# Kernel tuning notes

Measured on AMD Instinct MI355X. Metric: run time of the kernel, lower is better.

Reference implementation:

```python
import jax, jax.numpy as jnp
import numpy as np

WEIGHT_MSE = 1.0 / 3.0
W_DNA, W_RNA, W_LIG = 5.0, 5.0, 10.0
EPS = 1e-6


def _weighted_rigid_align(x, x_target, w):
    # x, x_target: [..., N, 3]; w: [..., N]. Aligns x onto x_target (Kabsch).
    w3 = w[..., None]                                   # [..., N, 1]
    wsum = jnp.sum(w, axis=-1, keepdims=True)[..., None]  # [..., 1, 1]
    mu_x = jnp.sum(w3 * x, axis=-2, keepdims=True) / wsum
    mu_t = jnp.sum(w3 * x_target, axis=-2, keepdims=True) / wsum
    xc = x - mu_x
    tc = x_target - mu_t
    # weighted covariance H = sum_n w_n * tc_n tc? -> [..., 3, 3]
    H = jnp.einsum('...ni,...nj->...ij', w3 * tc, xc)
    U, _, Vt = jnp.linalg.svd(H)
    d = jnp.sign(jnp.linalg.det(U @ Vt))                # reflection fix
    D = jnp.stack([jnp.ones_like(d), jnp.ones_like(d), d], axis=-1)
    R = (U * D[..., None, :]) @ Vt                      # [..., 3, 3]
    return jnp.einsum('...ij,...nj->...ni', R, xc) + mu_t


def setup_inputs() -> dict:
    key = jax.random.key(0)
    ks = jax.random.split(key, 7)
    B, S, N = 8, 48, 8192
    pred = jax.random.normal(ks[0], (B, S, N, 3), dtype=jnp.float32)
    true = jax.random.normal(ks[1], (B, N, 3), dtype=jnp.float32)
    mask = jax.random.randint(ks[2], (B, N), 0, 2, dtype=jnp.int32)
    is_dna = jax.random.randint(ks[3], (B, N), 0, 2, dtype=jnp.int32)
    is_rna = jax.random.randint(ks[4], (B, N), 0, 2, dtype=jnp.int32)
    is_lig = jax.random.randint(ks[5], (B, N), 0, 2, dtype=jnp.int32)
    scale = jax.random.uniform(ks[6], (B, S), dtype=jnp.float32)
    return {"pred_coordinate": pred, "true_coordinate": true,
            "coordinate_mask": mask, "is_dna": is_dna, "is_rna": is_rna,
            "is_ligand": is_lig, "per_sample_scale": scale}


def reference(pred_coordinate, true_coordinate, coordinate_mask, is_dna,
              is_rna, is_ligand, per_sample_scale):
    S = pred_coordinate.shape[-3]
    mask = coordinate_mask.astype(jnp.float32)          # [B, N]
    weight = (1.0 + W_DNA * is_dna.astype(jnp.float32)
              + W_RNA * is_rna.astype(jnp.float32)
              + W_LIG * is_ligand.astype(jnp.float32)) * mask
    true_m = true_coordinate * mask[..., None]          # [B, N, 3]
    pred_m = pred_coordinate * mask[..., None, :, None]  # [B, S, N, 3]
    true_e = jnp.broadcast_to(true_m[..., None, :, :], pred_coordinate.shape)
    weight_e = jnp.broadcast_to(weight[..., None, :],
                                pred_coordinate.shape[:-1])  # [B, S, N]
    aligned = jax.lax.stop_gradient(
        _weighted_rigid_align(true_e, pred_m, weight_e))
    weight_e = jax.lax.stop_gradient(weight_e)
    per_atom_se = jnp.sum((pred_coordinate - aligned) ** 2, axis=-1)  # [B,S,N]
    denom = jnp.sum(mask, axis=-1, keepdims=True) + EPS               # [B,1]
    per_sample = jnp.sum(weight_e * per_atom_se, axis=-1) / denom     # [B,S]
    per_sample = per_sample * per_sample_scale
    loss_b = WEIGHT_MSE * jnp.mean(per_sample, axis=-1)               # [B]
    return jnp.mean(loss_b)
```

## Files before the change

### kernel.cpp

```cpp
#include <hip/hip_runtime.h>
#include <math.h>

namespace {

constexpr int NB = 8;
constexpr int NS = 48;
constexpr int NA = 8192;
constexpr int BSIZE = 256;


template <int CNT>
__device__ inline void blockReduceWrite(const float (&v)[CNT], float* __restrict__ dst,
                                        float* lds, int nwaves) {
  const int lane = threadIdx.x & 63;
  const int wave = threadIdx.x >> 6;
#pragma unroll
  for (int k = 0; k < CNT; ++k) {
    float x = v[k];
#pragma unroll
    for (int off = 32; off; off >>= 1) x += __shfl_xor(x, off, 64);
    if (lane == 0) lds[wave * CNT + k] = x;
  }
  __syncthreads();
  if ((int)threadIdx.x < CNT) {
    float s = 0.f;
    for (int w = 0; w < nwaves; ++w) s += lds[w * CNT + threadIdx.x];
    dst[threadIdx.x] = s;
  }
}

__global__ __launch_bounds__(BSIZE) void reduce_kernel(
    const float* __restrict__ pred, const float* __restrict__ truec,
    const int* __restrict__ mask, const int* __restrict__ dna,
    const int* __restrict__ rna, const int* __restrict__ lig,
    float* __restrict__ ws) {
  __shared__ float lds[(BSIZE / 64) * 13];
  const int blk = blockIdx.x;

  if (blk < NB * NS) {
    const int b = blk / NS;
    const float* p = pred + (size_t)blk * NA * 3;
    const float* t = truec + (size_t)b * NA * 3;
    const int base = b * NA;

    float acc[13];
#pragma unroll
    for (int k = 0; k < 13; ++k) acc[k] = 0.f;

    auto atom = [&](float w, float p0, float p1, float p2, float t0, float t1, float t2) {
      const float w0 = w * p0, w1 = w * p1, w2 = w * p2;
      acc[0] += w0 * p0 + w1 * p1 + w2 * p2;
      acc[1] += w0;
      acc[2] += w1;
      acc[3] += w2;
      acc[4] += w0 * t0;
      acc[5] += w0 * t1;
      acc[6] += w0 * t2;
      acc[7] += w1 * t0;
      acc[8] += w1 * t1;
      acc[9] += w1 * t2;
      acc[10] += w2 * t0;
      acc[11] += w2 * t1;
      acc[12] += w2 * t2;
    };
    auto wgt = [](int m, int d, int r, int l) {
      return (1.0f + 5.0f * (float)d + 5.0f * (float)r + 10.0f * (float)l) * (float)m;
    };

    for (int it = 0; it < NA / (BSIZE * 4); ++it) {
      const int n0 = it * BSIZE * 4 + threadIdx.x * 4;
      const float4 pa = *(const float4*)(p + 3 * n0);
      const float4 pb = *(const float4*)(p + 3 * n0 + 4);
      const float4 pc = *(const float4*)(p + 3 * n0 + 8);
      const float4 ta = *(const float4*)(t + 3 * n0);
      const float4 tb = *(const float4*)(t + 3 * n0 + 4);
      const float4 tc = *(const float4*)(t + 3 * n0 + 8);
      const int4 mk = *(const int4*)(mask + base + n0);
      const int4 dn = *(const int4*)(dna + base + n0);
      const int4 rn = *(const int4*)(rna + base + n0);
      const int4 lg = *(const int4*)(lig + base + n0);

      atom(wgt(mk.x, dn.x, rn.x, lg.x), pa.x, pa.y, pa.z, ta.x, ta.y, ta.z);
      atom(wgt(mk.y, dn.y, rn.y, lg.y), pa.w, pb.x, pb.y, ta.w, tb.x, tb.y);
      atom(wgt(mk.z, dn.z, rn.z, lg.z), pb.z, pb.w, pc.x, tb.z, tb.w, tc.x);
      atom(wgt(mk.w, dn.w, rn.w, lg.w), pc.y, pc.z, pc.w, tc.y, tc.z, tc.w);
    }
    blockReduceWrite<13>(acc, ws + 64 + blk * 16, lds, BSIZE / 64);
  } else {
    const int b = blk - NB * NS;
    const float* t = truec + (size_t)b * NA * 3;
    const int base = b * NA;

    float acc[6];
#pragma unroll
    for (int k = 0; k < 6; ++k) acc[k] = 0.f;

    auto atomb = [&](int m, int d, int r, int l, float t0, float t1, float t2) {
      const float mf = (float)m;
      const float w = (1.0f + 5.0f * (float)d + 5.0f * (float)r + 10.0f * (float)l) * mf;
      acc[0] += w;
      acc[1] += w * t0;
      acc[2] += w * t1;
      acc[3] += w * t2;
      acc[4] += w * (t0 * t0 + t1 * t1 + t2 * t2);
      acc[5] += mf;
    };

    for (int it = 0; it < NA / (BSIZE * 4); ++it) {
      const int n0 = it * BSIZE * 4 + threadIdx.x * 4;
      const float4 ta = *(const float4*)(t + 3 * n0);
      const float4 tb = *(const float4*)(t + 3 * n0 + 4);
      const float4 tc = *(const float4*)(t + 3 * n0 + 8);
      const int4 mk = *(const int4*)(mask + base + n0);
      const int4 dn = *(const int4*)(dna + base + n0);
      const int4 rn = *(const int4*)(rna + base + n0);
      const int4 lg = *(const int4*)(lig + base + n0);

      atomb(mk.x, dn.x, rn.x, lg.x, ta.x, ta.y, ta.z);
      atomb(mk.y, dn.y, rn.y, lg.y, ta.w, tb.x, tb.y);
      atomb(mk.z, dn.z, rn.z, lg.z, tb.z, tb.w, tc.x);
      atomb(mk.w, dn.w, rn.w, lg.w, tc.y, tc.z, tc.w);
    }
    blockReduceWrite<6>(acc, ws + b * 8, lds, BSIZE / 64);
  }
}

__global__ __launch_bounds__(NB * NS) void final_kernel(const float* __restrict__ ws,
                                                        const float* __restrict__ scale,
                                                        float* __restrict__ out) {
  const int tid = threadIdx.x;
  const int b = tid / NS;

  const float* pb = ws + b * 8;
  const double wsum = (double)pb[0];
  const double st0 = (double)pb[1], st1 = (double)pb[2], st2 = (double)pb[3];
  const double stt = (double)pb[4];
  const double msum = (double)pb[5];

  const float* ps = ws + 64 + tid * 16;
  const double spp = (double)ps[0];
  const double sp0 = (double)ps[1], sp1 = (double)ps[2], sp2 = (double)ps[3];

  const double inv = 1.0 / wsum;
  const double Sp[3] = {sp0, sp1, sp2};
  const double St[3] = {st0, st1, st2};

  double H[3][3];
#pragma unroll
  for (int i = 0; i < 3; ++i)
#pragma unroll
    for (int j = 0; j < 3; ++j) H[i][j] = (double)ps[4 + 3 * i + j] - Sp[i] * St[j] * inv;

  const double Sq = spp - (sp0 * sp0 + sp1 * sp1 + sp2 * sp2) * inv;
  const double Sy = stt - (st0 * st0 + st1 * st1 + st2 * st2) * inv;

  double K[3][3];
#pragma unroll
  for (int i = 0; i < 3; ++i)
#pragma unroll
    for (int j = 0; j < 3; ++j)
      K[i][j] = H[0][i] * H[0][j] + H[1][i] * H[1][j] + H[2][i] * H[2][j];

  const double q = (K[0][0] + K[1][1] + K[2][2]) / 3.0;
  const double p1 = K[0][1] * K[0][1] + K[0][2] * K[0][2] + K[1][2] * K[1][2];
  const double a0 = K[0][0] - q, a1 = K[1][1] - q, a2 = K[2][2] - q;
  const double p2 = a0 * a0 + a1 * a1 + a2 * a2 + 2.0 * p1;
  double e1, e2, e3;
  if (p2 <= 1e-300) {
    e1 = e2 = e3 = q;
  } else {
    const double pp = sqrt(p2 / 6.0);
    const double ip = 1.0 / pp;
    const double B00 = a0 * ip, B11 = a1 * ip, B22 = a2 * ip;
    const double B01 = K[0][1] * ip, B02 = K[0][2] * ip, B12 = K[1][2] * ip;
    double r = 0.5 * (B00 * (B11 * B22 - B12 * B12) - B01 * (B01 * B22 - B12 * B02) +
                      B02 * (B01 * B12 - B11 * B02));
    r = fmin(1.0, fmax(-1.0, r));
    const double phi = acos(r) / 3.0;
    e1 = q + 2.0 * pp * cos(phi);
    e3 = q + 2.0 * pp * cos(phi + 2.0943951023931953);
    e2 = 3.0 * q - e1 - e3;
  }
  const double s1 = sqrt(fmax(e1, 0.0));
  const double s2 = sqrt(fmax(e2, 0.0));
  const double s3 = sqrt(fmax(e3, 0.0));

  const double detH =
      H[0][0] * (H[1][1] * H[2][2] - H[1][2] * H[2][1]) -
      H[0][1] * (H[1][0] * H[2][2] - H[1][2] * H[2][0]) +
      H[0][2] * (H[1][0] * H[2][1] - H[1][1] * H[2][0]);
  const double d = (detH > 0.0) ? 1.0 : ((detH < 0.0) ? -1.0 : 0.0);

  const double trRtH = s1 + s2 + d * s3;
  const double cost = Sq + Sy - 2.0 * trRtH;
  const double denom = msum + 1e-6;
  const double per_sample = cost / denom * (double)scale[tid];

  double c = per_sample * (1.0 / (3.0 * (double)NS * (double)NB));

#pragma unroll
  for (int off = 32; off; off >>= 1) c += __shfl_xor(c, off, 64);

  __shared__ double lds[NB * NS / 64];
  if ((tid & 63) == 0) lds[tid >> 6] = c;
  __syncthreads();
  if (tid == 0) {
    double s = 0.0;
    for (int w = 0; w < NB * NS / 64; ++w) s += lds[w];
    out[0] = (float)s;
  }
}

}

extern "C" void kernel_launch(void* const* d_in, const int* in_sizes, int n_in,
                              void* d_out, int out_size, void* d_ws, size_t ws_size,
                              hipStream_t stream) {
  const float* pred = (const float*)d_in[0];
  const float* truec = (const float*)d_in[1];
  const int* mask = (const int*)d_in[2];
  const int* dna = (const int*)d_in[3];
  const int* rna = (const int*)d_in[4];
  const int* lig = (const int*)d_in[5];
  const float* scale = (const float*)d_in[6];
  float* ws = (float*)d_ws;
  float* out = (float*)d_out;

  reduce_kernel<<<NB * NS + NB, BSIZE, 0, stream>>>(pred, truec, mask, dna, rna, lig, ws);
  final_kernel<<<1, NB * NS, 0, stream>>>(ws, scale, out);
}
```

Baseline: 23.95 us.

## Precompute per-atom weighted targets and split sample reductions into atom chunks

Adds a prep kernel that computes each atom's weight and weighted target (w, w·t) once per batch, stores them as packed float4 in the workspace, and reduces the per-batch target statistics in 64 blocks. The main kernel then reads pred plus the precomputed float4 instead of the target and four int masks. It also splits each sample's atom range into 4 chunks, giving 1536 blocks instead of 392 for better GPU occupancy. This costs one extra kernel launch, a workspace write/read round trip, and more partial sums to combine in the final kernel.

```diff
diff --git a/kernel.cpp b/kernel.cpp
--- a/kernel.cpp
+++ b/kernel.cpp
@@ -7,7 +7,11 @@
 constexpr int NS = 48;
 constexpr int NA = 8192;
 constexpr int BSIZE = 256;
-
+constexpr int CH = 4;
+
+constexpr int WT4 = 0;
+constexpr int PB = NB * NA * 4;
+constexpr int PS = PB + NB * 8 * 8;
 
 template <int CNT>
 __device__ inline void blockReduceWrite(const float (&v)[CNT], float* __restrict__ dst,
@@ -29,117 +33,135 @@
   }
 }
 
-__global__ __launch_bounds__(BSIZE) void reduce_kernel(
-    const float* __restrict__ pred, const float* __restrict__ truec,
-    const int* __restrict__ mask, const int* __restrict__ dna,
-    const int* __restrict__ rna, const int* __restrict__ lig,
-    float* __restrict__ ws) {
+__global__ __launch_bounds__(BSIZE) void prep_kernel(
+    const float* __restrict__ truec, const int* __restrict__ mask,
+    const int* __restrict__ dna, const int* __restrict__ rna,
+    const int* __restrict__ lig, float* __restrict__ ws) {
+  __shared__ float lds[(BSIZE / 64) * 6];
+  const int blk = blockIdx.x;
+  const int b = blk >> 3, j = blk & 7;
+  const int nloc = j * 1024 + threadIdx.x * 4;
+  const int gbase = b * NA + nloc;
+  const float* t = truec + (size_t)b * NA * 3 + 3 * nloc;
+
+  const float4 ta = *(const float4*)(t);
+  const float4 tb = *(const float4*)(t + 4);
+  const float4 tc = *(const float4*)(t + 8);
+  const int4 mk = *(const int4*)(mask + gbase);
+  const int4 dn = *(const int4*)(dna + gbase);
+  const int4 rn = *(const int4*)(rna + gbase);
+  const int4 lg = *(const int4*)(lig + gbase);
+
+  float acc[6];
+#pragma unroll
+  for (int k = 0; k < 6; ++k) acc[k] = 0.f;
+
+  auto one = [&](int idx, int m, int d, int r, int l, float t0, float t1, float t2) {
+    const float mf = (float)m;
+    const float w = (1.0f + 5.0f * (float)d + 5.0f * (float)r + 10.0f * (float)l) * mf;
+    const float4 o = make_float4(w, w * t0, w * t1, w * t2);
+    *(float4*)(ws + (size_t)(gbase + idx) * 4) = o;
+    acc[0] += w;
+    acc[1] += o.y;
+    acc[2] += o.z;
+    acc[3] += o.w;
+    acc[4] += w * (t0 * t0 + t1 * t1 + t2 * t2);
+    acc[5] += mf;
+  };
+
+  one(0, mk.x, dn.x, rn.x, lg.x, ta.x, ta.y, ta.z);
+  one(1, mk.y, dn.y, rn.y, lg.y, ta.w, tb.x, tb.y);
+  one(2, mk.z, dn.z, rn.z, lg.z, tb.z, tb.w, tc.x);
+  one(3, mk.w, dn.w, rn.w, lg.w, tc.y, tc.z, tc.w);
+
+  blockReduceWrite<6>(acc, ws + PB + blk * 8, lds, BSIZE / 64);
+}
+
+__global__ __launch_bounds__(BSIZE) void main_kernel(const float* __restrict__ pred,
+                                                     float* __restrict__ ws) {
   __shared__ float lds[(BSIZE / 64) * 13];
   const int blk = blockIdx.x;
-
-  if (blk < NB * NS) {
-    const int b = blk / NS;
-    const float* p = pred + (size_t)blk * NA * 3;
-    const float* t = truec + (size_t)b * NA * 3;
-    const int base = b * NA;
-
-    float acc[13];
-#pragma unroll
-    for (int k = 0; k < 13; ++k) acc[k] = 0.f;
-
-    auto atom = [&](float w, float p0, float p1, float p2, float t0, float t1, float t2) {
-      const float w0 = w * p0, w1 = w * p1, w2 = w * p2;
-      acc[0] += w0 * p0 + w1 * p1 + w2 * p2;
-      acc[1] += w0;
-      acc[2] += w1;
-      acc[3] += w2;
-      acc[4] += w0 * t0;
-      acc[5] += w0 * t1;
-      acc[6] += w0 * t2;
-      acc[7] += w1 * t0;
-      acc[8] += w1 * t1;
-      acc[9] += w1 * t2;
-      acc[10] += w2 * t0;
-      acc[11] += w2 * t1;
-      acc[12] += w2 * t2;
-    };
-    auto wgt = [](int m, int d, int r, int l) {
-      return (1.0f + 5.0f * (float)d + 5.0f * (float)r + 10.0f * (float)l) * (float)m;
-    };
-
-    for (int it = 0; it < NA / (BSIZE * 4); ++it) {
-      const int n0 = it * BSIZE * 4 + threadIdx.x * 4;
-      const float4 pa = *(const float4*)(p + 3 * n0);
-      const float4 pb = *(const float4*)(p + 3 * n0 + 4);
-      const float4 pc = *(const float4*)(p + 3 * n0 + 8);
-      const float4 ta = *(const float4*)(t + 3 * n0);
-      const float4 tb = *(const float4*)(t + 3 * n0 + 4);
-      const float4 tc = *(const float4*)(t + 3 * n0 + 8);
-      const int4 mk = *(const int4*)(mask + base + n0);
-      const int4 dn = *(const int4*)(dna + base + n0);
-      const int4 rn = *(const int4*)(rna + base + n0);
-      const int4 lg = *(const int4*)(lig + base + n0);
-
-      atom(wgt(mk.x, dn.x, rn.x, lg.x), pa.x, pa.y, pa.z, ta.x, ta.y, ta.z);
-      atom(wgt(mk.y, dn.y, rn.y, lg.y), pa.w, pb.x, pb.y, ta.w, tb.x, tb.y);
-      atom(wgt(mk.z, dn.z, rn.z, lg.z), pb.z, pb.w, pc.x, tb.z, tb.w, tc.x);
-      atom(wgt(mk.w, dn.w, rn.w, lg.w), pc.y, pc.z, pc.w, tc.y, tc.z, tc.w);
-    }
-    blockReduceWrite<13>(acc, ws + 64 + blk * 16, lds, BSIZE / 64);
-  } else {
-    const int b = blk - NB * NS;
-    const float* t = truec + (size_t)b * NA * 3;
-    const int base = b * NA;
-
-    float acc[6];
-#pragma unroll
-    for (int k = 0; k < 6; ++k) acc[k] = 0.f;
-
-    auto atomb = [&](int m, int d, int r, int l, float t0, float t1, float t2) {
-      const float mf = (float)m;
-      const float w = (1.0f + 5.0f * (float)d + 5.0f * (float)r + 10.0f * (float)l) * mf;
-      acc[0] += w;
-      acc[1] += w * t0;
-      acc[2] += w * t1;
-      acc[3] += w * t2;
-      acc[4] += w * (t0 * t0 + t1 * t1 + t2 * t2);
-      acc[5] += mf;
-    };
-
-    for (int it = 0; it < NA / (BSIZE * 4); ++it) {
-      const int n0 = it * BSIZE * 4 + threadIdx.x * 4;
-      const float4 ta = *(const float4*)(t + 3 * n0);
-      const float4 tb = *(const float4*)(t + 3 * n0 + 4);
-      const float4 tc = *(const float4*)(t + 3 * n0 + 8);
-      const int4 mk = *(const int4*)(mask + base + n0);
-      const int4 dn = *(const int4*)(dna + base + n0);
-      const int4 rn = *(const int4*)(rna + base + n0);
-      const int4 lg = *(const int4*)(lig + base + n0);
-
-      atomb(mk.x, dn.x, rn.x, lg.x, ta.x, ta.y, ta.z);
-      atomb(mk.y, dn.y, rn.y, lg.y, ta.w, tb.x, tb.y);
-      atomb(mk.z, dn.z, rn.z, lg.z, tb.z, tb.w, tc.x);
-      atomb(mk.w, dn.w, rn.w, lg.w, tc.y, tc.z, tc.w);
-    }
-    blockReduceWrite<6>(acc, ws + b * 8, lds, BSIZE / 64);
-  }
+  const int bs = blk / CH, chunk = blk % CH;
+  const int b = bs / NS;
+  const float* p = pred + (size_t)bs * NA * 3;
+  const float* wt = ws + (size_t)b * NA * 4;
+
+  float acc[13];
+#pragma unroll
+  for (int k = 0; k < 13; ++k) acc[k] = 0.f;
+
+  auto atom = [&](float4 q, float p0, float p1, float p2) {
+    const float wp0 = q.x * p0, wp1 = q.x * p1, wp2 = q.x * p2;
+    acc[0] += wp0 * p0 + wp1 * p1 + wp2 * p2;
+    acc[1] += wp0;
+    acc[2] += wp1;
+    acc[3] += wp2;
+    acc[4] += p0 * q.y;
+    acc[5] += p0 * q.z;
+    acc[6] += p0 * q.w;
+    acc[7] += p1 * q.y;
+    acc[8] += p1 * q.z;
+    acc[9] += p1 * q.w;
+    acc[10] += p2 * q.y;
+    acc[11] += p2 * q.z;
+    acc[12] += p2 * q.w;
+  };
+
+#pragma unroll
+  for (int it = 0; it < 2; ++it) {
+    const int n0 = chunk * 2048 + it * 1024 + threadIdx.x * 4;
+    const float4 pa = *(const float4*)(p + 3 * n0);
+    const float4 pb = *(const float4*)(p + 3 * n0 + 4);
+    const float4 pc = *(const float4*)(p + 3 * n0 + 8);
+    const float4 w0 = *(const float4*)(wt + (size_t)n0 * 4);
+    const float4 w1 = *(const float4*)(wt + (size_t)n0 * 4 + 4);
+    const float4 w2 = *(const float4*)(wt + (size_t)n0 * 4 + 8);
+    const float4 w3 = *(const float4*)(wt + (size_t)n0 * 4 + 12);
+
+    atom(w0, pa.x, pa.y, pa.z);
+    atom(w1, pa.w, pb.x, pb.y);
+    atom(w2, pb.z, pb.w, pc.x);
+    atom(w3, pc.y, pc.z, pc.w);
+  }
+
+  blockReduceWrite<13>(acc, ws + PS + blk * 16, lds, BSIZE / 64);
 }
 
 __global__ __launch_bounds__(NB * NS) void final_kernel(const float* __restrict__ ws,
                                                         const float* __restrict__ scale,
                                                         float* __restrict__ out) {
+  __shared__ double bvals[NB][6];
   const int tid = threadIdx.x;
+
+  if (tid < NB) {
+    double s[6] = {0, 0, 0, 0, 0, 0};
+    for (int jb = 0; jb < 8; ++jb) {
+      const float* q = ws + PB + (tid * 8 + jb) * 8;
+#pragma unroll
+      for (int k = 0; k < 6; ++k) s[k] += (double)q[k];
+    }
+#pragma unroll
+    for (int k = 0; k < 6; ++k) bvals[tid][k] = s[k];
+  }
+  __syncthreads();
+
   const int b = tid / NS;
-
-  const float* pb = ws + b * 8;
-  const double wsum = (double)pb[0];
-  const double st0 = (double)pb[1], st1 = (double)pb[2], st2 = (double)pb[3];
-  const double stt = (double)pb[4];
-  const double msum = (double)pb[5];
-
-  const float* ps = ws + 64 + tid * 16;
-  const double spp = (double)ps[0];
-  const double sp0 = (double)ps[1], sp1 = (double)ps[2], sp2 = (double)ps[3];
+  double sums[13];
+#pragma unroll
+  for (int k = 0; k < 13; ++k) sums[k] = 0.0;
+  for (int c = 0; c < CH; ++c) {
+    const float* q = ws + PS + (size_t)(tid * CH + c) * 16;
+#pragma unroll
+    for (int k = 0; k < 13; ++k) sums[k] += (double)q[k];
+  }
+
+  const double wsum = bvals[b][0];
+  const double st0 = bvals[b][1], st1 = bvals[b][2], st2 = bvals[b][3];
+  const double stt = bvals[b][4];
+  const double msum = bvals[b][5];
+
+  const double spp = sums[0];
+  const double sp0 = sums[1], sp1 = sums[2], sp2 = sums[3];
 
   const double inv = 1.0 / wsum;
   const double Sp[3] = {sp0, sp1, sp2};
@@ -149,7 +171,7 @@
 #pragma unroll
   for (int i = 0; i < 3; ++i)
 #pragma unroll
-    for (int j = 0; j < 3; ++j) H[i][j] = (double)ps[4 + 3 * i + j] - Sp[i] * St[j] * inv;
+    for (int j = 0; j < 3; ++j) H[i][j] = sums[4 + 3 * i + j] - Sp[i] * St[j] * inv;
 
   const double Sq = spp - (sp0 * sp0 + sp1 * sp1 + sp2 * sp2) * inv;
   const double Sy = stt - (st0 * st0 + st1 * st1 + st2 * st2) * inv;
@@ -226,6 +248,7 @@
   float* ws = (float*)d_ws;
   float* out = (float*)d_out;
 
-  reduce_kernel<<<NB * NS + NB, BSIZE, 0, stream>>>(pred, truec, mask, dna, rna, lig, ws);
+  prep_kernel<<<64, BSIZE, 0, stream>>>(truec, mask, dna, rna, lig, ws);
+  main_kernel<<<NB * NS * CH, BSIZE, 0, stream>>>(pred, ws);
   final_kernel<<<1, NB * NS, 0, stream>>>(ws, scale, out);
 }
```

After: 26.66 us. 1.11x slower.
